# Performance work log

Hardware: AMD Instinct MI355X
Metric: run time of the kernel (lower is better)

## Reference

```python
import jax, jax.numpy as jnp
import numpy as np
import math

N, B, S = 2048, 4, 1024
SFZ, IFZ, H, A = 384, 256, 8, 64
LN_EPS = 1e-5


def setup_inputs() -> dict:
    key = jax.random.key(0)
    ks = jax.random.split(key, 12)
    x = jax.random.normal(ks[0], (N, IFZ), dtype=jnp.float32)
    emb = jax.random.normal(ks[1], (B, S, SFZ), dtype=jnp.float32)
    mask = jax.random.randint(ks[2], (B, S), 0, 2).astype(bool)
    batch = jnp.sort(jax.random.randint(ks[3], (N,), 0, B)).astype(jnp.int64)
    sc = 1.0 / math.sqrt(IFZ)
    scs = 1.0 / math.sqrt(SFZ)
    Wq = jax.random.normal(ks[4], (IFZ, H * A), dtype=jnp.float32) * sc
    Wk = jax.random.normal(ks[5], (SFZ, H * A), dtype=jnp.float32) * scs
    Wv = jax.random.normal(ks[6], (SFZ, H * A), dtype=jnp.float32) * scs
    Wg = jax.random.normal(ks[7], (IFZ, H * A), dtype=jnp.float32) * sc
    bg = jnp.zeros((H * A,), dtype=jnp.float32)
    Wback = jax.random.normal(ks[8], (H * A, IFZ), dtype=jnp.float32) / math.sqrt(H * A)
    bback = jnp.zeros((IFZ,), dtype=jnp.float32)
    gamma = jnp.ones((IFZ,), dtype=jnp.float32)
    beta = jnp.zeros((IFZ,), dtype=jnp.float32)
    return {"x": x, "packed_sequence_emb": emb, "packed_sequence_mask": mask,
            "batch": batch, "Wq": Wq, "Wk": Wk, "Wv": Wv, "Wg": Wg, "bg": bg,
            "Wback": Wback, "bback": bback, "gamma": gamma, "beta": beta}


def _masked_softmax(scores, mask):
    # scores: [N,S,H], mask: [N,S,1] bool; softmax over S with padded entries zeroed
    neg = jnp.finfo(scores.dtype).min
    s = jnp.where(mask, scores, neg)
    s = s - jnp.max(s, axis=1, keepdims=True)
    e = jnp.exp(s) * mask
    return e / (jnp.sum(e, axis=1, keepdims=True) + 1e-9)


def reference(x, packed_sequence_emb, packed_sequence_mask, batch,
              Wq, Wk, Wv, Wg, bg, Wback, bback, gamma, beta):
    scale = math.sqrt(A)
    q = (x @ Wq).reshape(N, H, A)                               # [N,H,A]
    k = (packed_sequence_emb @ Wk).reshape(B, S, H, A)          # [B,S,H,A]
    v = (packed_sequence_emb @ Wv).reshape(B, S, H, A)
    # scores per (node, candidate-batch), then gather node's own batch entry;
    # avoids materializing k[batch] of shape [N,S,H,A]
    scores_all = jnp.einsum('nha,bsha->nbsh', q, k) / scale     # [N,B,S,H]
    idx = batch[:, None, None, None].astype(jnp.int32)
    scores = jnp.take_along_axis(scores_all, idx, axis=1)[:, 0]  # [N,S,H]
    bmask = packed_sequence_mask[batch][..., None]               # [N,S,1]
    w = _masked_softmax(scores, bmask)                           # [N,S,H]
    feat_all = jnp.einsum('nsh,bsha->nbha', w, v)                # [N,B,H,A]
    feat = jnp.take_along_axis(feat_all, idx, axis=1)[:, 0]      # [N,H,A]
    gate = jax.nn.sigmoid(x @ Wg + bg).reshape(N, H, A)
    new = (gate * feat).reshape(N, H * A) @ Wback + bback        # [N,IFZ]
    y = math.sqrt(2.0) * x + new
    mu = jnp.mean(y, axis=-1, keepdims=True)
    var = jnp.mean((y - mu) ** 2, axis=-1, keepdims=True)
    out = (y - mu) * jax.lax.rsqrt(var + LN_EPS) * gamma + beta
    seq_aa_logits = jnp.sum(scores[..., :2], axis=-1)            # [N,S]
    return out, seq_aa_logits
```

## Files before the change

kernel.cpp:

```cpp
#include <hip/hip_runtime.h>
#include <hip/hip_bf16.h>

#define NND 2048
#define BBATCH 4
#define SS 1024
#define SFZ 384
#define IFZ 256
#define HH 8
#define AA 64
#define HA 512
#define NBX 48
#define NSPL 8

typedef __attribute__((ext_vector_type(8))) short bf16x8;
typedef __attribute__((ext_vector_type(4))) float f32x4;

__device__ __forceinline__ unsigned short f2bf(float f) {
    union { float f; unsigned u; } a; a.f = f;
    unsigned r = a.u + 0x7fffu + ((a.u >> 16) & 1u);
    return (unsigned short)(r >> 16);
}
__device__ __forceinline__ float bf2f(unsigned short u) {
    return __uint_as_float((unsigned)u << 16);
}

__device__ __forceinline__ bf16x8 cvt8(const float* __restrict__ p) {
    const float4 f0 = *(const float4*)p;
    const float4 f1 = *(const float4*)(p + 4);
    bf16x8 o;
    o[0] = (short)f2bf(f0.x); o[1] = (short)f2bf(f0.y);
    o[2] = (short)f2bf(f0.z); o[3] = (short)f2bf(f0.w);
    o[4] = (short)f2bf(f1.x); o[5] = (short)f2bf(f1.y);
    o[6] = (short)f2bf(f1.z); o[7] = (short)f2bf(f1.w);
    return o;
}

__device__ __forceinline__ void tile_transpose(
    const float* __restrict__ src, unsigned short* __restrict__ dst,
    int K, int N, int kt, int nt, int t)
{
    __shared__ unsigned short tile[64][65];
    const int k0 = kt * 64, n0 = nt * 64;
    const int tr = t >> 6, tc = t & 63;
    #pragma unroll
    for (int r = 0; r < 16; ++r)
        tile[tr + r*4][tc] = f2bf(src[(size_t)(k0 + tr + r*4) * N + n0 + tc]);
    __syncthreads();
    #pragma unroll
    for (int r = 0; r < 16; ++r)
        dst[(size_t)(n0 + tr + r*4) * K + k0 + tc] = tile[tc][tr + r*4];
}

__global__ __launch_bounds__(256) void prep_kernel(
    const float* __restrict__ Wk, const float* __restrict__ Wv,
    const float* __restrict__ Wq, const float* __restrict__ Wg,
    const float* __restrict__ Wback,
    const void* __restrict__ mask_raw, const void* __restrict__ batch_raw,
    unsigned short* __restrict__ WkT, unsigned short* __restrict__ WvT,
    unsigned short* __restrict__ WqT, unsigned short* __restrict__ WgT,
    unsigned short* __restrict__ WbackT,
    float* __restrict__ mask_f, int* __restrict__ seg)
{
    const int bx = blockIdx.x, t = threadIdx.x;
    if (bx < 48)  { tile_transpose(Wk, WkT, SFZ, HA, bx/8, bx%8, t); return; }
    if (bx < 96)  { const int i = bx-48;  tile_transpose(Wv, WvT, SFZ, HA, i/8, i%8, t); return; }
    if (bx < 128) { const int i = bx-96;  tile_transpose(Wq, WqT, IFZ, HA, i/8, i%8, t); return; }
    if (bx < 160) { const int i = bx-128; tile_transpose(Wg, WgT, IFZ, HA, i/8, i%8, t); return; }
    if (bx < 192) { const int i = bx-160; tile_transpose(Wback, WbackT, HA, IFZ, i/4, i%4, t); return; }
    __shared__ int fl[4];
    __shared__ int fb;
    __shared__ int cnt[4];
    if (t < 4) { fl[t] = 0; cnt[t] = 0; }
    if (t == 0) fb = 0;
    __syncthreads();
    const unsigned char*  mb = (const unsigned char*)mask_raw;
    const unsigned short* mh = (const unsigned short*)mask_raw;
    const unsigned int*   mw = (const unsigned int*)mask_raw;
    int f0 = 0, f1 = 0, f2 = 0, f3 = 0;
    for (int i = t; i < 2048; i += 256) {
        unsigned short h = mh[i];
        if (h == 0x3f80u) f0 = 1;
        if ((i & 1) == 0 && h != 0) f1 = 1;
    }
    for (int i = t; i < 4096; i += 256)
        if ((i & 3) != 0 && mb[i] != 0) f2 = 1;
    for (int i = t; i < 1024; i += 256)
        if ((i & 1) != 0 && mw[i] != 0) f3 = 1;
    const int* bw = (const int*)batch_raw;
    int f4 = 0;
    for (int i = t + 1; i < 2048; i += 256)
        if (bw[i] < bw[i-1]) f4 = 1;
    if (f0) atomicOr(&fl[0], 1);
    if (f1) atomicOr(&fl[1], 1);
    if (f2) atomicOr(&fl[2], 1);
    if (f3) atomicOr(&fl[3], 1);
    if (f4) atomicOr(&fb, 1);
    __syncthreads();
    int mode;
    if (fl[0])      mode = fl[1] ? 1 : 0;
    else if (fl[2]) mode = 2;
    else if (fl[3]) mode = 3;
    else            mode = 4;
    for (int s = t; s < BBATCH*SS; s += 256) {
        int m;
        switch (mode) {
            case 0:  m = (mw[s]   != 0); break;
            case 1:  m = (mh[s]   != 0); break;
            case 2:  m = (mb[s]   != 0); break;
            case 3:  m = (mw[s]   != 0); break;
            default: m = (mw[2*s] != 0); break;
        }
        mask_f[s] = m ? 1.0f : 0.0f;
    }
    const int b64 = fb;
    for (int i = t; i < NND; i += 256) {
        const int bv = (b64 ? bw[2*i] : bw[i]) & 3;
        atomicAdd(&cnt[bv], 1);
    }
    __syncthreads();
    if (t == 0) {
        int s = 0;
        for (int b = 0; b < 4; ++b) { seg[2*b] = s; s += cnt[b]; seg[2*b+1] = s; }
    }
}

__global__ __launch_bounds__(256) void proj_mfma(
    const float* __restrict__ emb, const float* __restrict__ x,
    const unsigned short* __restrict__ WkT, const unsigned short* __restrict__ WvT,
    const unsigned short* __restrict__ WqT, const unsigned short* __restrict__ WgT,
    const float* __restrict__ bg,
    unsigned short* __restrict__ k_blk, unsigned short* __restrict__ vT_bf,
    unsigned short* __restrict__ q_bf, float* __restrict__ gate_ws)
{
    __shared__ unsigned short v_l[16][520];
    const int t = threadIdx.x, w = t >> 6, lane = t & 63;
    const int m16 = lane & 15, quad = lane >> 4;
    const int bx = blockIdx.x;
    if (bx < 512) {
        const int r0 = (bx >> 1) * 16;
        const int b = r0 >> 10, srow = r0 & (SS - 1);
        const float* ap = emb + (size_t)(r0 + m16) * SFZ + quad * 8;
        bf16x8 af[12];
        #pragma unroll
        for (int j = 0; j < 12; ++j) af[j] = cvt8(ap + j * 32);
        if ((bx & 1) == 0) {
            #pragma unroll
            for (int nt = 0; nt < 8; ++nt) {
                const int n0 = w * 128 + nt * 16;
                const unsigned short* bp = WkT + (size_t)(n0 + m16) * SFZ + quad * 8;
                f32x4 d = (f32x4){0.f, 0.f, 0.f, 0.f};
                #pragma unroll
                for (int j = 0; j < 12; ++j)
                    d = __builtin_amdgcn_mfma_f32_16x16x32_bf16(af[j], *(const bf16x8*)(bp + j * 32), d, 0, 0, 0);
                const int head = n0 >> 6, coff = (n0 & 63) + m16;
                unsigned short* kb = k_blk + (((size_t)(b * HH + head)) * SS) * 64 + coff;
                #pragma unroll
                for (int r = 0; r < 4; ++r)
                    kb[(size_t)(srow + quad * 4 + r) * 64] = f2bf(d[r]);
            }
        } else {
            #pragma unroll
            for (int nt = 0; nt < 8; ++nt) {
                const int n0 = w * 128 + nt * 16;
                const unsigned short* bp = WvT + (size_t)(n0 + m16) * SFZ + quad * 8;
                f32x4 d = (f32x4){0.f, 0.f, 0.f, 0.f};
                #pragma unroll
                for (int j = 0; j < 12; ++j)
                    d = __builtin_amdgcn_mfma_f32_16x16x32_bf16(af[j], *(const bf16x8*)(bp + j * 32), d, 0, 0, 0);
                #pragma unroll
                for (int r = 0; r < 4; ++r)
                    v_l[quad * 4 + r][n0 + m16] = f2bf(d[r]);
            }
            __syncthreads();
            for (int c = t; c < HA; c += 256) {
                unsigned short tmp[16];
                #pragma unroll
                for (int s = 0; s < 16; ++s) tmp[s] = v_l[s][c];
                unsigned short* dst = vT_bf + ((size_t)b * HA + c) * SS + srow;
                *(uint4*)dst       = ((const uint4*)tmp)[0];
                *(uint4*)(dst + 8) = ((const uint4*)tmp)[1];
            }
        }
    } else {
        const int i = bx - 512;
        const int r0 = (i >> 2) * 16;
        const int tensor = (i & 3) >> 1, half = i & 1;
        const unsigned short* Wt = tensor ? WgT : WqT;
        const float* ap = x + (size_t)(r0 + m16) * IFZ + quad * 8;
        bf16x8 af[8];
        #pragma unroll
        for (int j = 0; j < 8; ++j) af[j] = cvt8(ap + j * 32);
        #pragma unroll
        for (int nt = 0; nt < 4; ++nt) {
            const int n0 = half * 256 + w * 64 + nt * 16;
            const unsigned short* bp = Wt + (size_t)(n0 + m16) * IFZ + quad * 8;
            f32x4 d = (f32x4){0.f, 0.f, 0.f, 0.f};
            #pragma unroll
            for (int j = 0; j < 8; ++j)
                d = __builtin_amdgcn_mfma_f32_16x16x32_bf16(af[j], *(const bf16x8*)(bp + j * 32), d, 0, 0, 0);
            if (tensor == 0) {
                #pragma unroll
                for (int r = 0; r < 4; ++r)
                    q_bf[(size_t)(r0 + quad * 4 + r) * HA + n0 + m16] = f2bf(d[r]);
            } else {
                const float bgv = bg[n0 + m16];
                #pragma unroll
                for (int r = 0; r < 4; ++r)
                    gate_ws[(size_t)(r0 + quad * 4 + r) * HA + n0 + m16] =
                        1.f / (1.f + __expf(-(d[r] + bgv)));
            }
        }
    }
}

__global__ __launch_bounds__(256) void attn_kernel(
    const unsigned short* __restrict__ k_blk, const unsigned short* __restrict__ vT_bf,
    const unsigned short* __restrict__ q_bf, const float* __restrict__ mask_f,
    const int* __restrict__ seg, unsigned short* __restrict__ part_O,
    float2* __restrict__ part_ml, float* __restrict__ out_logits)
{
    __shared__ unsigned short P_lds[4][16][136];
    __shared__ float raw[2][16][132];
    const int bid = blockIdx.x;
    const int xcd = bid & 7;
    const int b   = xcd >> 1;
    const int idx = (bid >> 3) * 2 + (xcd & 1);
    const int z    = idx & 15;
    const int xblk = idx >> 4;
    const int hz    = z >> 3;
    const int split = z & 7;
    const int n0 = seg[2*b] + xblk * 16;
    const int nend = seg[2*b + 1];
    if (n0 >= nend) return;
    const int nvalid = min(16, nend - n0);

    const int t = threadIdx.x;
    const int w = t >> 6, lane = t & 63;
    const int m16 = lane & 15, quad = lane >> 4;
    const int h = hz * 4 + w;
    const int s0 = split * 128;

    int nq = n0 + m16; if (nq >= nend) nq = nend - 1;
    const unsigned short* qp = q_bf + (size_t)nq * HA + h * AA + quad * 8;
    const bf16x8 qa0 = *(const bf16x8*)qp;
    const bf16x8 qa1 = *(const bf16x8*)(qp + 32);

    const unsigned short* kb = k_blk + ((size_t)(b * HH + h)) * SS * 64;
    const unsigned short* vb = vT_bf + ((size_t)b * HA + h * AA) * SS;
    unsigned short (*Pw)[136] = P_lds[w];

    float msk[8];
    #pragma unroll
    for (int st = 0; st < 8; ++st)
        msk[st] = mask_f[b * SS + s0 + st * 16 + m16];

    f32x4 d[8];
    #pragma unroll
    for (int st = 0; st < 8; ++st) {
        const unsigned short* kp = kb + (size_t)(s0 + st * 16 + m16) * 64 + quad * 8;
        const bf16x8 b0 = *(const bf16x8*)kp;
        const bf16x8 b1 = *(const bf16x8*)(kp + 32);
        f32x4 acc = (f32x4){0.f, 0.f, 0.f, 0.f};
        acc = __builtin_amdgcn_mfma_f32_16x16x32_bf16(qa0, b0, acc, 0, 0, 0);
        acc = __builtin_amdgcn_mfma_f32_16x16x32_bf16(qa1, b1, acc, 0, 0, 0);
        #pragma unroll
        for (int r = 0; r < 4; ++r) acc[r] *= 0.125f;
        d[st] = acc;
    }
    if (hz == 0) {
        if (w < 2) {
            #pragma unroll
            for (int st = 0; st < 8; ++st)
                #pragma unroll
                for (int r = 0; r < 4; ++r)
                    raw[w][quad * 4 + r][st * 16 + m16] = d[st][r];
        }
        __syncthreads();
        for (int i = t; i < 16 * 128; i += 256) {
            const int node = i >> 7, sp = i & 127;
            if (node < nvalid)
                out_logits[(size_t)(n0 + node) * SS + s0 + sp] =
                    raw[0][node][sp] + raw[1][node][sp];
        }
    }
    float m_s[4], l_s[4];
    #pragma unroll
    for (int r = 0; r < 4; ++r) {
        float mx = -3.0e38f;
        #pragma unroll
        for (int st = 0; st < 8; ++st)
            mx = (msk[st] > 0.5f) ? fmaxf(mx, d[st][r]) : mx;
        mx = fmaxf(mx, __shfl_xor(mx, 1));
        mx = fmaxf(mx, __shfl_xor(mx, 2));
        mx = fmaxf(mx, __shfl_xor(mx, 4));
        mx = fmaxf(mx, __shfl_xor(mx, 8));
        m_s[r] = mx;
        float cs = 0.f;
        #pragma unroll
        for (int st = 0; st < 8; ++st) {
            const float e = (msk[st] > 0.5f) ? __expf(d[st][r] - mx) : 0.f;
            d[st][r] = e;
            cs += e;
        }
        cs += __shfl_xor(cs, 1);
        cs += __shfl_xor(cs, 2);
        cs += __shfl_xor(cs, 4);
        cs += __shfl_xor(cs, 8);
        l_s[r] = cs;
    }
    #pragma unroll
    for (int st = 0; st < 8; ++st)
        #pragma unroll
        for (int r = 0; r < 4; ++r)
            Pw[quad * 4 + r][st * 16 + m16] = f2bf(d[st][r]);
    f32x4 facc[4];
    #pragma unroll
    for (int a = 0; a < 4; ++a) facc[a] = (f32x4){0.f, 0.f, 0.f, 0.f};
    #pragma unroll
    for (int sub = 0; sub < 4; ++sub) {
        const bf16x8 pa = *(const bf16x8*)&Pw[m16][sub * 32 + quad * 8];
        const unsigned short* vp0 = vb + (size_t)m16 * SS + s0 + sub * 32 + quad * 8;
        #pragma unroll
        for (int a = 0; a < 4; ++a) {
            const bf16x8 vfr = *(const bf16x8*)(vp0 + (size_t)(a * 16) * SS);
            facc[a] = __builtin_amdgcn_mfma_f32_16x16x32_bf16(pa, vfr, facc[a], 0, 0, 0);
        }
    }
    unsigned short* po = part_O + (size_t)split * NND * HA;
    #pragma unroll
    for (int a = 0; a < 4; ++a)
        #pragma unroll
        for (int r = 0; r < 4; ++r) {
            const int row = quad * 4 + r;
            if (row < nvalid)
                po[(size_t)(n0 + row) * HA + h * AA + a * 16 + m16] = f2bf(facc[a][r]);
        }
    if (m16 == 0) {
        #pragma unroll
        for (int r = 0; r < 4; ++r) {
            const int row = quad * 4 + r;
            if (row < nvalid)
                part_ml[(size_t)split * NND * HH + (size_t)(n0 + row) * HH + h] =
                    make_float2(m_s[r], l_s[r]);
        }
    }
}

__global__ __launch_bounds__(256) void back_ln_fused(
    const unsigned short* __restrict__ part_O, const float2* __restrict__ part_ml,
    const float* __restrict__ gate_ws, const unsigned short* __restrict__ WbackT,
    const float* __restrict__ x, const float* __restrict__ bback,
    const float* __restrict__ gamma, const float* __restrict__ beta,
    float* __restrict__ out)
{
    __shared__ float coef[NSPL][8][8];
    __shared__ unsigned short gf_l[8][520];
    __shared__ float nl[8][260];
    const int t = threadIdx.x, w = t >> 6, lane = t & 63;
    const int m16 = lane & 15, quad = lane >> 4;
    const int r0 = blockIdx.x * 8;
    if (t < 64) {
        const int row = t >> 3, h = t & 7, n = r0 + row;
        float2 ml[NSPL];
        #pragma unroll
        for (int s = 0; s < NSPL; ++s)
            ml[s] = part_ml[(size_t)s * NND * HH + (size_t)n * HH + h];
        float M = -3.0e38f;
        #pragma unroll
        for (int s = 0; s < NSPL; ++s) M = fmaxf(M, ml[s].x);
        float L = 0.f;
        float e[NSPL];
        #pragma unroll
        for (int s = 0; s < NSPL; ++s) { e[s] = __expf(ml[s].x - M); L += ml[s].y * e[s]; }
        const float invL = 1.f / (L + 1e-9f);
        #pragma unroll
        for (int s = 0; s < NSPL; ++s) coef[s][row][h] = e[s] * invL;
    }
    __syncthreads();
    #pragma unroll
    for (int it = 0; it < 4; ++it) {
        const int i = (t + it * 256) * 4;
        const int row = i >> 9, c = i & (HA - 1), h = c >> 6;
        const int n = r0 + row;
        float4 o = make_float4(0.f, 0.f, 0.f, 0.f);
        #pragma unroll
        for (int s = 0; s < NSPL; ++s) {
            const ushort4 p = *(const ushort4*)&part_O[(size_t)s * NND * HA + (size_t)n * HA + c];
            const float cf = coef[s][row][h];
            o.x = fmaf(bf2f(p.x), cf, o.x); o.y = fmaf(bf2f(p.y), cf, o.y);
            o.z = fmaf(bf2f(p.z), cf, o.z); o.w = fmaf(bf2f(p.w), cf, o.w);
        }
        const float4 g = *(const float4*)&gate_ws[(size_t)n * HA + c];
        ushort4 ob;
        ob.x = f2bf(g.x * o.x); ob.y = f2bf(g.y * o.y);
        ob.z = f2bf(g.z * o.z); ob.w = f2bf(g.w * o.w);
        *(ushort4*)&gf_l[row][c] = ob;
    }
    __syncthreads();
    bf16x8 af[16];
    #pragma unroll
    for (int j = 0; j < 16; ++j)
        af[j] = *(const bf16x8*)&gf_l[m16 & 7][quad * 8 + j * 32];
    #pragma unroll
    for (int nt = 0; nt < 4; ++nt) {
        const int n0 = w * 64 + nt * 16;
        const unsigned short* bp = WbackT + (size_t)(n0 + m16) * HA + quad * 8;
        f32x4 d = (f32x4){0.f, 0.f, 0.f, 0.f};
        #pragma unroll
        for (int j = 0; j < 16; ++j)
            d = __builtin_amdgcn_mfma_f32_16x16x32_bf16(af[j], *(const bf16x8*)(bp + j * 32), d, 0, 0, 0);
        const float bb = bback[n0 + m16];
        #pragma unroll
        for (int r = 0; r < 4; ++r) {
            const int rr = quad * 4 + r;
            if (rr < 8) nl[rr][n0 + m16] = d[r] + bb;
        }
    }
    __syncthreads();
    const int row = t >> 5, li = t & 31;
    const float* xr = x + (size_t)(r0 + row) * IFZ;
    float yv[8];
    float s1 = 0.f, s2 = 0.f;
    #pragma unroll
    for (int j = 0; j < 8; ++j) {
        const int c = li + j * 32;
        const float v = fmaf(1.41421356237309515f, xr[c], nl[row][c]);
        yv[j] = v; s1 += v; s2 += v * v;
    }
    #pragma unroll
    for (int off = 16; off >= 1; off >>= 1) {
        s1 += __shfl_xor(s1, off);
        s2 += __shfl_xor(s2, off);
    }
    const float mu  = s1 * (1.f / IFZ);
    const float var = s2 * (1.f / IFZ) - mu * mu;
    const float rv  = rsqrtf(var + 1e-5f);
    float* orow = out + (size_t)(r0 + row) * IFZ;
    #pragma unroll
    for (int j = 0; j < 8; ++j) {
        const int c = li + j * 32;
        orow[c] = (yv[j] - mu) * rv * gamma[c] + beta[c];
    }
}

extern "C" void kernel_launch(void* const* d_in, const int* in_sizes, int n_in,
                              void* d_out, int out_size, void* d_ws, size_t ws_size,
                              hipStream_t stream) {
    const float* x     = (const float*)d_in[0];
    const float* emb   = (const float*)d_in[1];
    const void*  mraw  = d_in[2];
    const void*  braw  = d_in[3];
    const float* Wq    = (const float*)d_in[4];
    const float* Wk    = (const float*)d_in[5];
    const float* Wv    = (const float*)d_in[6];
    const float* Wg    = (const float*)d_in[7];
    const float* bg    = (const float*)d_in[8];
    const float* Wback = (const float*)d_in[9];
    const float* bback = (const float*)d_in[10];
    const float* gamma = (const float*)d_in[11];
    const float* beta  = (const float*)d_in[12];

    char* ws = (char*)d_ws;
    const size_t MB = 1048576;
    size_t off = 0;
    float*          mask_f  = (float*)(ws + off);  off += 16384;
    int*            seg     = (int*)(ws + off);    off += 16384;
    unsigned short* WkT     = (unsigned short*)(ws + off); off += 393216;
    unsigned short* WvT     = (unsigned short*)(ws + off); off += 393216;
    unsigned short* WqT     = (unsigned short*)(ws + off); off += 262144;
    unsigned short* WgT     = (unsigned short*)(ws + off); off += 262144;
    unsigned short* WbackT  = (unsigned short*)(ws + off); off += 262144;
    unsigned short* k_blk   = (unsigned short*)(ws + off); off += 4*MB;
    unsigned short* vT_bf   = (unsigned short*)(ws + off); off += 4*MB;
    unsigned short* q_bf    = (unsigned short*)(ws + off); off += 2*MB;
    float*          gate_ws = (float*)(ws + off); off += 4*MB;
    unsigned short* part_O  = (unsigned short*)(ws + off); off += 16*MB;
    float2*         part_ml = (float2*)(ws + off); off += 1*MB;

    float* out        = (float*)d_out;
    float* out_logits = out + (size_t)NND * IFZ;

    hipLaunchKernelGGL(prep_kernel, dim3(193), dim3(256), 0, stream,
                       Wk, Wv, Wq, Wg, Wback, mraw, braw,
                       WkT, WvT, WqT, WgT, WbackT, mask_f, seg);
    hipLaunchKernelGGL(proj_mfma, dim3(1024), dim3(256), 0, stream,
                       emb, x, WkT, WvT, WqT, WgT, bg, k_blk, vT_bf, q_bf, gate_ws);
    hipLaunchKernelGGL(attn_kernel, dim3(BBATCH * NBX * 16), dim3(256), 0, stream,
                       k_blk, vT_bf, q_bf, mask_f, seg, part_O, part_ml, out_logits);
    hipLaunchKernelGGL(back_ln_fused, dim3(NND / 8), dim3(256), 0, stream,
                       part_O, part_ml, gate_ws, WbackT, x, bback, gamma, beta, out);
}
```

Baseline: 198.5 us.

## Fuse split-combine, back projection and layernorm into attention via last-block ticket

Removes the separate back_ln_fused launch. Each attention block bumps a per-(batch, node-tile) atomic ticket after writing its partial output, and the last of the 16 blocks for that tile combines the split partials, applies the gate, runs the Wback MFMA and the layernorm. Shared memory is reused through a union. This saves a kernel launch and a full pass over the partials, but the tail work is serialized onto a few last-arriving blocks and adds fences and atomics. The ticket counters are zeroed in prep_kernel.

```diff
diff --git a/kernel.cpp b/kernel.cpp
--- a/kernel.cpp
+++ b/kernel.cpp
@@ -59,7 +59,7 @@
     unsigned short* __restrict__ WkT, unsigned short* __restrict__ WvT,
     unsigned short* __restrict__ WqT, unsigned short* __restrict__ WgT,
     unsigned short* __restrict__ WbackT,
-    float* __restrict__ mask_f, int* __restrict__ seg)
+    float* __restrict__ mask_f, int* __restrict__ seg, int* __restrict__ ticket)
 {
     const int bx = blockIdx.x, t = threadIdx.x;
     if (bx < 48)  { tile_transpose(Wk, WkT, SFZ, HA, bx/8, bx%8, t); return; }
@@ -72,6 +72,7 @@
     __shared__ int cnt[4];
     if (t < 4) { fl[t] = 0; cnt[t] = 0; }
     if (t == 0) fb = 0;
+    if (t < BBATCH * NBX) ticket[t] = 0;
     __syncthreads();
     const unsigned char*  mb = (const unsigned char*)mask_raw;
     const unsigned short* mh = (const unsigned short*)mask_raw;
@@ -213,14 +214,24 @@
     }
 }
 
+union AttnSMem {
+    struct { unsigned short P[4][16][136]; float raw[2][16][132]; } a;
+    struct { float coef[NSPL][16][8]; unsigned short gf[16][520];
+             float nl[16][260]; } f;
+};
+
 __global__ __launch_bounds__(256) void attn_kernel(
     const unsigned short* __restrict__ k_blk, const unsigned short* __restrict__ vT_bf,
     const unsigned short* __restrict__ q_bf, const float* __restrict__ mask_f,
     const int* __restrict__ seg, unsigned short* __restrict__ part_O,
-    float2* __restrict__ part_ml, float* __restrict__ out_logits)
+    float2* __restrict__ part_ml, float* __restrict__ out_logits,
+    const float* __restrict__ gate_ws, const unsigned short* __restrict__ WbackT,
+    const float* __restrict__ x, const float* __restrict__ bback,
+    const float* __restrict__ gamma, const float* __restrict__ beta,
+    float* __restrict__ out, int* __restrict__ ticket)
 {
-    __shared__ unsigned short P_lds[4][16][136];
-    __shared__ float raw[2][16][132];
+    __shared__ AttnSMem sm;
+    __shared__ int lastf;
     const int bid = blockIdx.x;
     const int xcd = bid & 7;
     const int b   = xcd >> 1;
@@ -247,7 +258,7 @@
 
     const unsigned short* kb = k_blk + ((size_t)(b * HH + h)) * SS * 64;
     const unsigned short* vb = vT_bf + ((size_t)b * HA + h * AA) * SS;
-    unsigned short (*Pw)[136] = P_lds[w];
+    unsigned short (*Pw)[136] = sm.a.P[w];
 
     float msk[8];
     #pragma unroll
@@ -273,14 +284,14 @@
             for (int st = 0; st < 8; ++st)
                 #pragma unroll
                 for (int r = 0; r < 4; ++r)
-                    raw[w][quad * 4 + r][st * 16 + m16] = d[st][r];
+                    sm.a.raw[w][quad * 4 + r][st * 16 + m16] = d[st][r];
         }
         __syncthreads();
         for (int i = t; i < 16 * 128; i += 256) {
             const int node = i >> 7, sp = i & 127;
             if (node < nvalid)
                 out_logits[(size_t)(n0 + node) * SS + s0 + sp] =
-                    raw[0][node][sp] + raw[1][node][sp];
+                    sm.a.raw[0][node][sp] + sm.a.raw[1][node][sp];
         }
     }
     float m_s[4], l_s[4];
@@ -344,27 +355,21 @@
                     make_float2(m_s[r], l_s[r]);
         }
     }
-}
-
-__global__ __launch_bounds__(256) void back_ln_fused(
-    const unsigned short* __restrict__ part_O, const float2* __restrict__ part_ml,
-    const float* __restrict__ gate_ws, const unsigned short* __restrict__ WbackT,
-    const float* __restrict__ x, const float* __restrict__ bback,
-    const float* __restrict__ gamma, const float* __restrict__ beta,
-    float* __restrict__ out)
-{
-    __shared__ float coef[NSPL][8][8];
-    __shared__ unsigned short gf_l[8][520];
-    __shared__ float nl[8][260];
-    const int t = threadIdx.x, w = t >> 6, lane = t & 63;
-    const int m16 = lane & 15, quad = lane >> 4;
-    const int r0 = blockIdx.x * 8;
-    if (t < 64) {
-        const int row = t >> 3, h = t & 7, n = r0 + row;
+
+    __threadfence();
+    __syncthreads();
+    if (t == 0) lastf = (atomicAdd(&ticket[b * NBX + xblk], 1) == 15);
+    __syncthreads();
+    if (!lastf) return;
+    __threadfence();
+
+    if (t < 128) {
+        const int row = t >> 3, hh = t & 7;
+        const int n = min(n0 + row, NND - 1);
         float2 ml[NSPL];
         #pragma unroll
         for (int s = 0; s < NSPL; ++s)
-            ml[s] = part_ml[(size_t)s * NND * HH + (size_t)n * HH + h];
+            ml[s] = part_ml[(size_t)s * NND * HH + (size_t)n * HH + hh];
         float M = -3.0e38f;
         #pragma unroll
         for (int s = 0; s < NSPL; ++s) M = fmaxf(M, ml[s].x);
@@ -374,19 +379,19 @@
         for (int s = 0; s < NSPL; ++s) { e[s] = __expf(ml[s].x - M); L += ml[s].y * e[s]; }
         const float invL = 1.f / (L + 1e-9f);
         #pragma unroll
-        for (int s = 0; s < NSPL; ++s) coef[s][row][h] = e[s] * invL;
-    }
-    __syncthreads();
-    #pragma unroll
-    for (int it = 0; it < 4; ++it) {
+        for (int s = 0; s < NSPL; ++s) sm.f.coef[s][row][hh] = e[s] * invL;
+    }
+    __syncthreads();
+    #pragma unroll
+    for (int it = 0; it < 8; ++it) {
         const int i = (t + it * 256) * 4;
-        const int row = i >> 9, c = i & (HA - 1), h = c >> 6;
-        const int n = r0 + row;
+        const int row = i >> 9, c = i & (HA - 1), hh = c >> 6;
+        const int n = min(n0 + row, NND - 1);
         float4 o = make_float4(0.f, 0.f, 0.f, 0.f);
         #pragma unroll
         for (int s = 0; s < NSPL; ++s) {
             const ushort4 p = *(const ushort4*)&part_O[(size_t)s * NND * HA + (size_t)n * HA + c];
-            const float cf = coef[s][row][h];
+            const float cf = sm.f.coef[s][row][hh];
             o.x = fmaf(bf2f(p.x), cf, o.x); o.y = fmaf(bf2f(p.y), cf, o.y);
             o.z = fmaf(bf2f(p.z), cf, o.z); o.w = fmaf(bf2f(p.w), cf, o.w);
         }
@@ -394,52 +399,50 @@
         ushort4 ob;
         ob.x = f2bf(g.x * o.x); ob.y = f2bf(g.y * o.y);
         ob.z = f2bf(g.z * o.z); ob.w = f2bf(g.w * o.w);
-        *(ushort4*)&gf_l[row][c] = ob;
-    }
-    __syncthreads();
-    bf16x8 af[16];
-    #pragma unroll
-    for (int j = 0; j < 16; ++j)
-        af[j] = *(const bf16x8*)&gf_l[m16 & 7][quad * 8 + j * 32];
+        *(ushort4*)&sm.f.gf[row][c] = ob;
+    }
+    __syncthreads();
     #pragma unroll
     for (int nt = 0; nt < 4; ++nt) {
-        const int n0 = w * 64 + nt * 16;
-        const unsigned short* bp = WbackT + (size_t)(n0 + m16) * HA + quad * 8;
-        f32x4 d = (f32x4){0.f, 0.f, 0.f, 0.f};
-        #pragma unroll
-        for (int j = 0; j < 16; ++j)
-            d = __builtin_amdgcn_mfma_f32_16x16x32_bf16(af[j], *(const bf16x8*)(bp + j * 32), d, 0, 0, 0);
-        const float bb = bback[n0 + m16];
-        #pragma unroll
-        for (int r = 0; r < 4; ++r) {
-            const int rr = quad * 4 + r;
-            if (rr < 8) nl[rr][n0 + m16] = d[r] + bb;
-        }
-    }
-    __syncthreads();
-    const int row = t >> 5, li = t & 31;
-    const float* xr = x + (size_t)(r0 + row) * IFZ;
-    float yv[8];
-    float s1 = 0.f, s2 = 0.f;
-    #pragma unroll
-    for (int j = 0; j < 8; ++j) {
-        const int c = li + j * 32;
-        const float v = fmaf(1.41421356237309515f, xr[c], nl[row][c]);
-        yv[j] = v; s1 += v; s2 += v * v;
-    }
-    #pragma unroll
-    for (int off = 16; off >= 1; off >>= 1) {
-        s1 += __shfl_xor(s1, off);
-        s2 += __shfl_xor(s2, off);
-    }
-    const float mu  = s1 * (1.f / IFZ);
-    const float var = s2 * (1.f / IFZ) - mu * mu;
-    const float rv  = rsqrtf(var + 1e-5f);
-    float* orow = out + (size_t)(r0 + row) * IFZ;
-    #pragma unroll
-    for (int j = 0; j < 8; ++j) {
-        const int c = li + j * 32;
-        orow[c] = (yv[j] - mu) * rv * gamma[c] + beta[c];
+        const int nc = w * 64 + nt * 16;
+        const unsigned short* bp = WbackT + (size_t)(nc + m16) * HA + quad * 8;
+        f32x4 dd = (f32x4){0.f, 0.f, 0.f, 0.f};
+        #pragma unroll
+        for (int j = 0; j < 16; ++j) {
+            const bf16x8 afj = *(const bf16x8*)&sm.f.gf[m16][quad * 8 + j * 32];
+            dd = __builtin_amdgcn_mfma_f32_16x16x32_bf16(afj, *(const bf16x8*)(bp + j * 32), dd, 0, 0, 0);
+        }
+        const float bb = bback[nc + m16];
+        #pragma unroll
+        for (int r = 0; r < 4; ++r)
+            sm.f.nl[quad * 4 + r][nc + m16] = dd[r] + bb;
+    }
+    __syncthreads();
+    {
+        const int row = t >> 4, c0 = t & 15;
+        const int n = min(n0 + row, NND - 1);
+        const float* xr = x + (size_t)n * IFZ;
+        float yv[16];
+        float s1 = 0.f, s2 = 0.f;
+        #pragma unroll
+        for (int j = 0; j < 16; ++j) {
+            const float v = fmaf(1.41421356237309515f, xr[c0 + j * 16], sm.f.nl[row][c0 + j * 16]);
+            yv[j] = v; s1 += v; s2 += v * v;
+        }
+        #pragma unroll
+        for (int off = 8; off >= 1; off >>= 1) {
+            s1 += __shfl_xor(s1, off);
+            s2 += __shfl_xor(s2, off);
+        }
+        const float mu  = s1 * (1.f / IFZ);
+        const float var = s2 * (1.f / IFZ) - mu * mu;
+        const float rv  = rsqrtf(var + 1e-5f);
+        if (row < nvalid) {
+            float* orow = out + (size_t)(n0 + row) * IFZ;
+            #pragma unroll
+            for (int j = 0; j < 16; ++j)
+                orow[c0 + j * 16] = (yv[j] - mu) * rv * gamma[c0 + j * 16] + beta[c0 + j * 16];
+        }
     }
 }
 
@@ -464,7 +467,8 @@
     const size_t MB = 1048576;
     size_t off = 0;
     float*          mask_f  = (float*)(ws + off);  off += 16384;
-    int*            seg     = (int*)(ws + off);    off += 16384;
+    int*            seg     = (int*)(ws + off);
+    int*            ticket  = (int*)(ws + off + 4096);  off += 16384;
     unsigned short* WkT     = (unsigned short*)(ws + off); off += 393216;
     unsigned short* WvT     = (unsigned short*)(ws + off); off += 393216;
     unsigned short* WqT     = (unsigned short*)(ws + off); off += 262144;
@@ -482,11 +486,10 @@
 
     hipLaunchKernelGGL(prep_kernel, dim3(193), dim3(256), 0, stream,
                        Wk, Wv, Wq, Wg, Wback, mraw, braw,
-                       WkT, WvT, WqT, WgT, WbackT, mask_f, seg);
+                       WkT, WvT, WqT, WgT, WbackT, mask_f, seg, ticket);
     hipLaunchKernelGGL(proj_mfma, dim3(1024), dim3(256), 0, stream,
                        emb, x, WkT, WvT, WqT, WgT, bg, k_blk, vT_bf, q_bf, gate_ws);
     hipLaunchKernelGGL(attn_kernel, dim3(BBATCH * NBX * 16), dim3(256), 0, stream,
-                       k_blk, vT_bf, q_bf, mask_f, seg, part_O, part_ml, out_logits);
-    hipLaunchKernelGGL(back_ln_fused, dim3(NND / 8), dim3(256), 0, stream,
-                       part_O, part_ml, gate_ws, WbackT, x, bback, gamma, beta, out);
-}
+                       k_blk, vT_bf, q_bf, mask_f, seg, part_O, part_ml, out_logits,
+                       gate_ws, WbackT, x, bback, gamma, beta, out, ticket);
+}
```

Result: slower. 533.4 us (+168.6%).
